# Kernel tuning notes

Measured on AMD Instinct MI355X. Metric: run time of the kernel, lower is better.

Reference implementation:

```python
import jax, jax.numpy as jnp
import numpy as np

B = 2; N_RAW = 16384; N_KP = 2048; M_VOX = 8192; C_VOX = 64
H_BEV, W_BEV, C_BEV, BEV_STRIDE = 200, 176, 256, 8
VOXEL_SIZE = np.array([0.05, 0.05, 0.1], np.float32)
PC_MIN = np.array([0.0, -40.0, -3.0], np.float32)
DOWNSAMPLE = 4
RAW_RADII = (0.4, 0.8); RAW_NS = (16, 16)
CONV_RADII = (1.2, 2.4); CONV_NS = (16, 32)
BN_SCALE = float(1.0 / np.sqrt(1.0 + 1e-5))  # eval-mode BN, running mean=0 var=1


def _fps_idx(pts, n):
    # farthest point sampling over pts [N,3] -> [n] int32 indices
    N = pts.shape[0]
    def step(carry, _):
        dists, last = carry
        d = jnp.sum((pts - pts[last]) ** 2, axis=-1)
        dists = jnp.minimum(dists, d)
        nxt = jnp.argmax(dists).astype(jnp.int32)
        return (dists, nxt), nxt
    init = (jnp.full((N,), 1e10, pts.dtype), jnp.int32(0))
    _, rest = jax.lax.scan(step, init, None, length=n - 1)
    return jnp.concatenate([jnp.zeros((1,), jnp.int32), rest])


def _bilinear(bev, x, y):
    # bev [H,W,C]; faithful to bilinear_interpolate_bev (clamp then weight)
    H, W, _ = bev.shape
    xf = jnp.floor(x); yf = jnp.floor(y)
    x0 = jnp.clip(xf.astype(jnp.int32), 0, W - 1)
    x1 = jnp.clip(xf.astype(jnp.int32) + 1, 0, W - 1)
    y0 = jnp.clip(yf.astype(jnp.int32), 0, H - 1)
    y1 = jnp.clip(yf.astype(jnp.int32) + 1, 0, H - 1)
    fa = bev[y1, x0]; fb = bev[y1, x1]; fc = bev[y0, x1]; fd = bev[y0, x0]
    x0f = x0.astype(x.dtype); x1f = x1.astype(x.dtype)
    y0f = y0.astype(y.dtype); y1f = y1.astype(y.dtype)
    wa = (x - x0f) * (y1f - y); wb = (x1f - x) * (y1f - y)
    wc = (x1f - x) * (y - y0f); wd = (x - x0f) * (y - y0f)
    return fd * wb[:, None] + fc * wa[:, None] + fa * wc[:, None] + fb * wd[:, None]


def _group(xyz, feats, new_xyz, radius, nsample):
    # ball query: first nsample points within radius (original order), pad with first hit
    M = xyz.shape[0]
    d2 = jnp.sum((new_xyz[:, None, :] - xyz[None, :, :]) ** 2, axis=-1)  # [K,M]
    mask = d2 < radius * radius
    key = jnp.where(mask, jnp.arange(M, dtype=jnp.int32)[None, :], M)
    idx = jnp.sort(key, axis=1)[:, :nsample]
    empty = ~jnp.any(mask, axis=1)
    idx = jnp.where(idx < M, idx, idx[:, :1])
    idx = jnp.clip(idx, 0, M - 1)
    g_xyz = xyz[idx] - new_xyz[:, None, :]
    g = jnp.concatenate([g_xyz, feats[idx]], axis=-1)  # [K,ns,3+C]
    return jnp.where(empty[:, None, None], 0.0, g), empty


def _bn_relu(x, g, b):
    return jax.nn.relu(x * (g * BN_SCALE) + b)


def _sa(xyz, feats, new_xyz, radii, nss, w0, g0, b0, w1, g1, b1):
    outs = []
    for i, (r, ns) in enumerate(zip(radii, nss)):
        grouped, empty = jax.vmap(lambda x, f, nx: _group(x, f, nx, r, ns))(xyz, feats, new_xyz)
        h = _bn_relu(grouped @ w0[i], g0[i], b0[i])
        h = _bn_relu(h @ w1[i], g1[i], b1[i])
        pooled = jnp.max(h, axis=2)  # [B,K,Cout]
        outs.append(jnp.where(empty[..., None], 0.0, pooled))
    return jnp.concatenate(outs, axis=-1)


def _forward(points, spatial_features, voxel_coords, voxel_features,
             raw_w0, raw_g0, raw_b0, raw_w1, raw_g1, raw_b1,
             conv_w0, conv_g0, conv_b0, conv_w1, conv_g1, conv_b1,
             fusion_w, fusion_g, fusion_b):
    pts = points.reshape(B, N_RAW, -1)
    xyz_raw = pts[..., 1:4]
    idxs = jax.vmap(lambda p: _fps_idx(p, N_KP))(jax.lax.stop_gradient(xyz_raw))
    kp = jnp.take_along_axis(xyz_raw, idxs[..., None], axis=1)  # [B,NKP,3]
    xi = (kp[..., 0] - PC_MIN[0]) / VOXEL_SIZE[0] / BEV_STRIDE
    yi = (kp[..., 1] - PC_MIN[1]) / VOXEL_SIZE[1] / BEV_STRIDE
    bev = jnp.transpose(spatial_features, (0, 2, 3, 1))  # [B,H,W,C]
    bev_feat = jax.vmap(_bilinear)(bev, xi, yi)  # [B,NKP,C_BEV]
    raw_feat = _sa(xyz_raw, pts[..., 4:], kp, RAW_RADII, RAW_NS,
                   raw_w0, raw_g0, raw_b0, raw_w1, raw_g1, raw_b1)
    vc = voxel_coords.reshape(B, M_VOX, 4)
    centers = (vc[..., jnp.array([3, 2, 1])].astype(jnp.float32) + 0.5) \
        * jnp.asarray(VOXEL_SIZE * DOWNSAMPLE) + jnp.asarray(PC_MIN)
    conv_feat = _sa(centers, voxel_features.reshape(B, M_VOX, C_VOX), kp, CONV_RADII, CONV_NS,
                    conv_w0, conv_g0, conv_b0, conv_w1, conv_g1, conv_b1)
    feats = jnp.concatenate([bev_feat, raw_feat, conv_feat], axis=-1).reshape(B * N_KP, -1)
    return _bn_relu(feats @ fusion_w, fusion_g, fusion_b)  # [B*NKP, 128]


def setup_inputs():
    key = jax.random.key(0)
    ks = jax.random.split(key, 8)
    xyz = jax.random.uniform(ks[0], (B * N_RAW, 3), jnp.float32) * jnp.array([70.4, 80.0, 4.0]) + jnp.array([0.0, -40.0, -3.0])
    inten = jax.random.uniform(ks[1], (B * N_RAW, 1), jnp.float32)
    bidx = jnp.repeat(jnp.arange(B, dtype=jnp.float32), N_RAW)[:, None]
    points = jnp.concatenate([bidx, xyz, inten], axis=1)
    spatial_features = jax.random.normal(ks[2], (B, C_BEV, H_BEV, W_BEV), jnp.float32)
    vb = jnp.repeat(jnp.arange(B, dtype=jnp.int32), M_VOX)[:, None]
    vz = jax.random.randint(ks[3], (B * M_VOX, 1), 0, 10, jnp.int32)
    vy = jax.random.randint(ks[4], (B * M_VOX, 1), 0, 400, jnp.int32)
    vx = jax.random.randint(ks[5], (B * M_VOX, 1), 0, 352, jnp.int32)
    voxel_coords = jnp.concatenate([vb, vz, vy, vx], axis=1)
    voxel_features = jax.random.normal(ks[6], (B * M_VOX, C_VOX), jnp.float32)
    pk = jax.random.split(ks[7], 5)
    w = lambda k, s: jax.random.normal(k, s, jnp.float32) * 0.05
    return dict(
        points=points, spatial_features=spatial_features,
        voxel_coords=voxel_coords, voxel_features=voxel_features,
        raw_w0=w(pk[0], (2, 4, 16)), raw_g0=jnp.ones((2, 16)), raw_b0=jnp.zeros((2, 16)),
        raw_w1=w(pk[1], (2, 16, 16)), raw_g1=jnp.ones((2, 16)), raw_b1=jnp.zeros((2, 16)),
        conv_w0=w(pk[2], (2, 67, 64)), conv_g0=jnp.ones((2, 64)), conv_b0=jnp.zeros((2, 64)),
        conv_w1=w(pk[3], (2, 64, 64)), conv_g1=jnp.ones((2, 64)), conv_b1=jnp.zeros((2, 64)),
        fusion_w=w(pk[4], (416, 128)), fusion_g=jnp.ones((128,)), fusion_b=jnp.zeros((128,)))


def reference(points, spatial_features, voxel_coords, voxel_features,
              raw_w0, raw_g0, raw_b0, raw_w1, raw_g1, raw_b1,
              conv_w0, conv_g0, conv_b0, conv_w1, conv_g1, conv_b1,
              fusion_w, fusion_g, fusion_b):
    return _forward(points, spatial_features, voxel_coords, voxel_features,
                    raw_w0, raw_g0, raw_b0, raw_w1, raw_g1, raw_b1,
                    conv_w0, conv_g0, conv_b0, conv_w1, conv_g1, conv_b1,
                    fusion_w, fusion_g, fusion_b)
```

## Files before the change

kernel.cpp:

```cpp
#include <hip/hip_runtime.h>


#define NRAW   16384
#define MVOX   8192
#define NKP    2048
#define NKPALL 4096

__device__ __constant__ float kBNS = (float)0.9999950000374997;

typedef float f32x2 __attribute__((ext_vector_type(2)));

__global__ __launch_bounds__(256) void prep_kernel(
    const float* __restrict__ pts, const int* __restrict__ vc,
    float4* __restrict__ xyz4, float4* __restrict__ cxyz4) {
#pragma clang fp contract(off)
  int i = blockIdx.x * 256 + threadIdx.x;
  if (i < 2 * NRAW) {
    const float* p = pts + (size_t)i * 5;
    xyz4[i] = make_float4(p[1], p[2], p[3], p[4]);
  }
  if (i < 2 * MVOX) {
    const int* v = vc + (size_t)i * 4;
    cxyz4[i] = make_float4(((float)v[3] + 0.5f) * 0.2f + 0.0f,
                           ((float)v[2] + 0.5f) * 0.2f + -40.0f,
                           ((float)v[1] + 0.5f) * 0.4f + -3.0f, 0.f);
  }
}

__global__ __launch_bounds__(1024) void sort_kernel(
    const float* __restrict__ pts, int* __restrict__ sperm) {
  const int b = blockIdx.x, t = threadIdx.x;
  __shared__ unsigned hist[256], cur[256];
  if (t < 256) hist[t] = 0u;
  __syncthreads();
  int bins[16];
#pragma unroll
  for (int k = 0; k < 16; ++k) {
    const int i = k * 1024 + t;
    const float y = pts[(size_t)(b * NRAW + i) * 5 + 2];
    int bin = (int)((y + 40.0f) * 3.2f);
    bin = bin < 0 ? 0 : (bin > 255 ? 255 : bin);
    bins[k] = bin;
    atomicAdd(&hist[bin], 1u);
  }
  __syncthreads();
  if (t == 0) {
    unsigned acc = 0;
    for (int i = 0; i < 256; ++i) { cur[i] = acc; acc += hist[i]; }
  }
  __syncthreads();
#pragma unroll
  for (int k = 0; k < 16; ++k) {
    const int i = k * 1024 + t;
    const unsigned pos = atomicAdd(&cur[bins[k]], 1u);
    sperm[b * NRAW + pos] = i;
  }
}

#define U64_STAGE(CTRL, RMASK)                                                 \
  {                                                                            \
    const unsigned tlo = (unsigned)__builtin_amdgcn_update_dpp(                \
        0, (int)lo, CTRL, RMASK, 0xf, true);                                   \
    const unsigned thi = (unsigned)__builtin_amdgcn_update_dpp(                \
        0, (int)hi, CTRL, RMASK, 0xf, true);                                   \
    const unsigned long long tv = ((unsigned long long)thi << 32) | tlo;       \
    const unsigned long long cv = ((unsigned long long)hi << 32) | lo;         \
    if (tv > cv) { hi = thi; lo = tlo; }                                       \
  }

__global__ __launch_bounds__(1024, 4) void fps_kernel(
    const int* __restrict__ sperm, const float4* __restrict__ xyz4,
    float* __restrict__ kx, float* __restrict__ ky, float* __restrict__ kz) {
#pragma clang fp contract(off)
  const int b = blockIdx.x;
  const int t = threadIdx.x;
  const int w = t >> 6, lane = t & 63;
  const int wb = w * 1024;
  const int base = b * NRAW;

  __shared__ unsigned long long slot[3];

  int pj[16];
  f32x2 px2[8], py2[8], pz2[8], dd2[8];
#pragma unroll
  for (int j = 0; j < 16; ++j)
    pj[j] = sperm[base + wb + j * 64 + lane];
#pragma unroll
  for (int j = 0; j < 16; ++j) {
    const float4 q = xyz4[base + pj[j]];
    px2[j >> 1][j & 1] = q.x;
    py2[j >> 1][j & 1] = q.y;
    pz2[j >> 1][j & 1] = q.z;
    dd2[j >> 1][j & 1] = 1e10f;
  }
  if (t < 3) slot[t] = 0ULL;

  float bnx = px2[0].x, bxx = px2[0].x, bny = py2[0].x, bxy = py2[0].x,
        bnz = pz2[0].x, bxz = pz2[0].x;
#pragma unroll
  for (int j = 1; j < 16; ++j) {
    bnx = fminf(bnx, px2[j >> 1][j & 1]); bxx = fmaxf(bxx, px2[j >> 1][j & 1]);
    bny = fminf(bny, py2[j >> 1][j & 1]); bxy = fmaxf(bxy, py2[j >> 1][j & 1]);
    bnz = fminf(bnz, pz2[j >> 1][j & 1]); bxz = fmaxf(bxz, pz2[j >> 1][j & 1]);
  }
#pragma unroll
  for (int off = 1; off < 64; off <<= 1) {
    bnx = fminf(bnx, __shfl_xor(bnx, off, 64));
    bxx = fmaxf(bxx, __shfl_xor(bxx, off, 64));
    bny = fminf(bny, __shfl_xor(bny, off, 64));
    bxy = fmaxf(bxy, __shfl_xor(bxy, off, 64));
    bnz = fminf(bnz, __shfl_xor(bnz, off, 64));
    bxz = fmaxf(bxz, __shfl_xor(bxz, off, 64));
  }

  const float4 p0 = xyz4[base];
  float lx = p0.x, ly = p0.y, lz = p0.z;
  if (t == 0) { kx[b * NKP] = lx; ky[b * NKP] = ly; kz[b * NKP] = lz; }

  unsigned long long cpk = 0ULL;
  float bvc = __builtin_inff();
  __syncthreads();

  for (int s = 1; s < NKP; ++s) {
    float dxm = fmaxf(fmaxf(bnx - lx, lx - bxx), 0.f);
    float dym = fmaxf(fmaxf(bny - ly, ly - bxy), 0.f);
    float dzm = fmaxf(fmaxf(bnz - lz, lz - bxz), 0.f);
    const float LB2 = dxm * dxm + dym * dym + dzm * dzm;
    if (!(LB2 * 0.9999f > bvc)) {
      const f32x2 lx2 = {lx, lx}, ly2 = {ly, ly}, lz2 = {lz, lz};
#pragma unroll
      for (int j8 = 0; j8 < 8; ++j8) {
        f32x2 dx = px2[j8] - lx2;
        f32x2 dy = py2[j8] - ly2;
        f32x2 dz = pz2[j8] - lz2;
        f32x2 d2 = dx * dx;
        d2 = d2 + dy * dy;
        d2 = d2 + dz * dz;
        dd2[j8] = __builtin_elementwise_min(dd2[j8], d2);
      }
      f32x2 t0 = __builtin_elementwise_max(dd2[0], dd2[1]);
      f32x2 t1 = __builtin_elementwise_max(dd2[2], dd2[3]);
      f32x2 t2 = __builtin_elementwise_max(dd2[4], dd2[5]);
      f32x2 t3 = __builtin_elementwise_max(dd2[6], dd2[7]);
      t0 = __builtin_elementwise_max(t0, t1);
      t2 = __builtin_elementwise_max(t2, t3);
      t0 = __builtin_elementwise_max(t0, t2);
      const float bv = fmaxf(t0.x, t0.y);
      const unsigned vb = __float_as_uint(bv);
      unsigned mo = 0xFFFFFFFFu;
#pragma unroll
      for (int j = 0; j < 16; ++j)
        if (__float_as_uint(dd2[j >> 1][j & 1]) == vb) {
          const unsigned o = (unsigned)pj[j];
          mo = o < mo ? o : mo;
        }
      unsigned hi = vb, lo = ~mo;
      U64_STAGE(0xB1,  0xf)
      U64_STAGE(0x4E,  0xf)
      U64_STAGE(0x124, 0xf)
      U64_STAGE(0x128, 0xf)
      U64_STAGE(0x142, 0xa)
      U64_STAGE(0x143, 0xc)
      bvc = __uint_as_float(
          (unsigned)__builtin_amdgcn_readlane((int)hi, 63));
      cpk = ((unsigned long long)hi << 32) | (unsigned long long)lo;
    }
    if (lane == 63) atomicMax(&slot[s % 3], cpk);
    __syncthreads();

    const unsigned long long g = slot[s % 3];
    const int wi = __builtin_amdgcn_readfirstlane((int)~(unsigned)g);
    if (t == 0) slot[(s + 2) % 3] = 0ULL;
    const float4 cw = xyz4[base + wi];
    lx = cw.x; ly = cw.y; lz = cw.z;
    if (t == 0) { kx[b * NKP + s] = lx; ky[b * NKP + s] = ly; kz[b * NKP + s] = lz; }
  }
}

__global__ __launch_bounds__(256) void bev_kernel(
    const float* __restrict__ sf, const float* __restrict__ kx,
    const float* __restrict__ ky, float* __restrict__ feats) {
#pragma clang fp contract(off)
  const int kidx = blockIdx.x;
  const int c = threadIdx.x;
  const int b = kidx >> 11;
  const float x = (kx[kidx] - 0.0f) / 0.05f / 8.0f;
  const float y = (ky[kidx] - (-40.0f)) / 0.05f / 8.0f;
  const float xf = floorf(x), yf = floorf(y);
  int x0 = (int)xf;     x0 = x0 < 0 ? 0 : (x0 > 175 ? 175 : x0);
  int x1 = (int)xf + 1; x1 = x1 < 0 ? 0 : (x1 > 175 ? 175 : x1);
  int y0 = (int)yf;     y0 = y0 < 0 ? 0 : (y0 > 199 ? 199 : y0);
  int y1 = (int)yf + 1; y1 = y1 < 0 ? 0 : (y1 > 199 ? 199 : y1);
  const float x0f = (float)x0, x1f = (float)x1, y0f = (float)y0, y1f = (float)y1;
  const float wa = (x - x0f) * (y1f - y);
  const float wb = (x1f - x) * (y1f - y);
  const float wc = (x1f - x) * (y - y0f);
  const float wd = (x - x0f) * (y - y0f);
  const float* base = sf + ((size_t)b * 256 + c) * (200 * 176);
  const float fa = base[y1 * 176 + x0];
  const float fb = base[y1 * 176 + x1];
  const float fc = base[y0 * 176 + x1];
  const float fd = base[y0 * 176 + x0];
  float r = fd * wb; r = r + fc * wa; r = r + fa * wc; r = r + fb * wd;
  feats[(size_t)kidx * 416 + c] = r;
}

__global__ __launch_bounds__(256) void raw_sa_kernel(
    const float4* __restrict__ xyz4,
    const float* __restrict__ kx, const float* __restrict__ ky,
    const float* __restrict__ kz,
    const float* __restrict__ w0, const float* __restrict__ g0,
    const float* __restrict__ b0, const float* __restrict__ w1,
    const float* __restrict__ g1, const float* __restrict__ b1,
    float* __restrict__ feats) {
  const int wv = threadIdx.x >> 6;
  const int lane = threadIdx.x & 63;
  const int gw = blockIdx.x * 4 + wv;
  const int ri = gw >> 12;
  const int kidx = gw & 4095;
  const int b = kidx >> 11;
  const float R2 = ri ? (float)(0.8 * 0.8) : (float)(0.4 * 0.4);

  __shared__ int   idxl[4][16];
  __shared__ float hbuf[4][16][17];

  const float kxv = kx[kidx], kyv = ky[kidx], kzv = kz[kidx];
  const int base = b * NRAW;
  int cnt = 0;
  {
#pragma clang fp contract(off)
    for (int ch = 0; ch < NRAW / 64 && cnt < 16; ++ch) {
      const float4 q = xyz4[base + ch * 64 + lane];
      float dx = kxv - q.x, dy = kyv - q.y, dz = kzv - q.z;
      float d2 = dx * dx; d2 = d2 + dy * dy; d2 = d2 + dz * dz;
      unsigned long long m = __ballot(d2 < R2);
      while (m && cnt < 16) {
        int bit = __builtin_ctzll(m);
        if (lane == 0) idxl[wv][cnt] = ch * 64 + bit;
        ++cnt;
        m &= m - 1;
      }
    }
  }
  const int outoff = kidx * 416 + 256 + ri * 16;
  if (cnt == 0) {
    if (lane < 16) feats[outoff + lane] = 0.f;
    return;
  }
  __threadfence_block();

  const int s = lane & 15, cq = lane >> 4;
  const int ss = (s < cnt) ? s : 0;
  const float4 q = xyz4[base + idxl[wv][ss]];
  const float gx = q.x - kxv, gy = q.y - kyv, gz = q.z - kzv, gi = q.w;
  const int wb0 = ri * 64, cb = ri * 16;
#pragma unroll
  for (int j = 0; j < 4; ++j) {
    int c = cq * 4 + j;
    float a = gx * w0[wb0 + c];
    a = fmaf(gy, w0[wb0 + 16 + c], a);
    a = fmaf(gz, w0[wb0 + 32 + c], a);
    a = fmaf(gi, w0[wb0 + 48 + c], a);
    a = fmaf(a, g0[cb + c] * kBNS, b0[cb + c]);
    hbuf[wv][s][c] = fmaxf(a, 0.f);
  }
  __threadfence_block();
  float o0 = 0.f, o1 = 0.f, o2 = 0.f, o3 = 0.f;
  const int wb1 = ri * 256;
#pragma unroll
  for (int k = 0; k < 16; ++k) {
    float hk = hbuf[wv][s][k];
    o0 = fmaf(hk, w1[wb1 + k * 16 + cq * 4 + 0], o0);
    o1 = fmaf(hk, w1[wb1 + k * 16 + cq * 4 + 1], o1);
    o2 = fmaf(hk, w1[wb1 + k * 16 + cq * 4 + 2], o2);
    o3 = fmaf(hk, w1[wb1 + k * 16 + cq * 4 + 3], o3);
  }
  float v0 = fmaxf(fmaf(o0, g1[cb + cq * 4 + 0] * kBNS, b1[cb + cq * 4 + 0]), 0.f);
  float v1 = fmaxf(fmaf(o1, g1[cb + cq * 4 + 1] * kBNS, b1[cb + cq * 4 + 1]), 0.f);
  float v2 = fmaxf(fmaf(o2, g1[cb + cq * 4 + 2] * kBNS, b1[cb + cq * 4 + 2]), 0.f);
  float v3 = fmaxf(fmaf(o3, g1[cb + cq * 4 + 3] * kBNS, b1[cb + cq * 4 + 3]), 0.f);
#pragma unroll
  for (int off = 1; off < 16; off <<= 1) {
    v0 = fmaxf(v0, __shfl_xor(v0, off, 64));
    v1 = fmaxf(v1, __shfl_xor(v1, off, 64));
    v2 = fmaxf(v2, __shfl_xor(v2, off, 64));
    v3 = fmaxf(v3, __shfl_xor(v3, off, 64));
  }
  if (s == 0) {
    feats[outoff + cq * 4 + 0] = v0;
    feats[outoff + cq * 4 + 1] = v1;
    feats[outoff + cq * 4 + 2] = v2;
    feats[outoff + cq * 4 + 3] = v3;
  }
}

__global__ __launch_bounds__(256) void conv_sa_kernel(
    const float4* __restrict__ cxyz4, const float* __restrict__ vf,
    const float* __restrict__ kx, const float* __restrict__ ky,
    const float* __restrict__ kz,
    const float* __restrict__ w0, const float* __restrict__ g0,
    const float* __restrict__ b0, const float* __restrict__ w1,
    const float* __restrict__ g1, const float* __restrict__ b1,
    float* __restrict__ feats) {
  const int wv = threadIdx.x >> 6;
  const int lane = threadIdx.x & 63;
  const int gw = blockIdx.x * 4 + wv;
  const int ri = gw >> 12;
  const int kidx = gw & 4095;
  const int b = kidx >> 11;
  const int NS = ri ? 32 : 16;
  const float R2 = ri ? (float)(2.4 * 2.4) : (float)(1.2 * 1.2);

  __shared__ int   idxl[4][32];
  __shared__ float gbuf[4][64];
  __shared__ float hbuf[4][32][64];

  const float kxv = kx[kidx], kyv = ky[kidx], kzv = kz[kidx];
  const int base = b * MVOX;
  int cnt = 0;
  {
#pragma clang fp contract(off)
    for (int ch = 0; ch < MVOX / 64 && cnt < NS; ++ch) {
      const float4 q = cxyz4[base + ch * 64 + lane];
      float dx = kxv - q.x, dy = kyv - q.y, dz = kzv - q.z;
      float d2 = dx * dx; d2 = d2 + dy * dy; d2 = d2 + dz * dz;
      unsigned long long m = __ballot(d2 < R2);
      while (m && cnt < NS) {
        int bit = __builtin_ctzll(m);
        if (lane == 0) idxl[wv][cnt] = ch * 64 + bit;
        ++cnt;
        m &= m - 1;
      }
    }
  }
  const int outoff = kidx * 416 + 288 + ri * 64;
  if (cnt == 0) {
    feats[outoff + lane] = 0.f;
    return;
  }
  __threadfence_block();

  const float wA0 = w0[(ri * 67 + 0) * 64 + lane];
  const float wA1 = w0[(ri * 67 + 1) * 64 + lane];
  const float wA2 = w0[(ri * 67 + 2) * 64 + lane];
  float wB[64];
#pragma unroll
  for (int k = 0; k < 64; ++k) wB[k] = w0[(ri * 67 + 3 + k) * 64 + lane];
  float wC[64];
#pragma unroll
  for (int k = 0; k < 64; ++k) wC[k] = w1[(ri * 64 + k) * 64 + lane];
  const float s0 = g0[ri * 64 + lane] * kBNS, bb0 = b0[ri * 64 + lane];
  const float s1 = g1[ri * 64 + lane] * kBNS, bb1 = b1[ri * 64 + lane];

  for (int sm = 0; sm < cnt; ++sm) {
    const int p = base + idxl[wv][sm];
    const float4 q = cxyz4[p];
    const float ox = q.x - kxv, oy = q.y - kyv, oz = q.z - kzv;
    gbuf[wv][lane] = vf[(size_t)p * 64 + lane];
    __threadfence_block();
    float acc = ox * wA0;
    acc = fmaf(oy, wA1, acc);
    acc = fmaf(oz, wA2, acc);
#pragma unroll
    for (int k4 = 0; k4 < 16; ++k4) {
      float4 g4 = *(const float4*)&gbuf[wv][k4 * 4];
      acc = fmaf(g4.x, wB[k4 * 4 + 0], acc);
      acc = fmaf(g4.y, wB[k4 * 4 + 1], acc);
      acc = fmaf(g4.z, wB[k4 * 4 + 2], acc);
      acc = fmaf(g4.w, wB[k4 * 4 + 3], acc);
    }
    hbuf[wv][sm][lane] = fmaxf(fmaf(acc, s0, bb0), 0.f);
    __threadfence_block();
  }
  float mx = -1e30f;
  for (int sm = 0; sm < cnt; ++sm) {
    float acc = 0.f;
#pragma unroll
    for (int k4 = 0; k4 < 16; ++k4) {
      float4 h4 = *(const float4*)&hbuf[wv][sm][k4 * 4];
      acc = fmaf(h4.x, wC[k4 * 4 + 0], acc);
      acc = fmaf(h4.y, wC[k4 * 4 + 1], acc);
      acc = fmaf(h4.z, wC[k4 * 4 + 2], acc);
      acc = fmaf(h4.w, wC[k4 * 4 + 3], acc);
    }
    mx = fmaxf(mx, fmaxf(fmaf(acc, s1, bb1), 0.f));
  }
  feats[outoff + lane] = mx;
}

__global__ __launch_bounds__(256) void fusion_kernel(
    const float* __restrict__ feats, const float* __restrict__ fw,
    const float* __restrict__ fg, const float* __restrict__ fb,
    float* __restrict__ out) {
  const int gid = blockIdx.x * 256 + threadIdx.x;
  const int kidx = gid >> 7, c = gid & 127;
  const float* f = feats + (size_t)kidx * 416;
  float acc = 0.f;
#pragma unroll 4
  for (int k = 0; k < 416; k += 4) {
    float4 fv = *(const float4*)(f + k);
    acc = fmaf(fv.x, fw[(k + 0) * 128 + c], acc);
    acc = fmaf(fv.y, fw[(k + 1) * 128 + c], acc);
    acc = fmaf(fv.z, fw[(k + 2) * 128 + c], acc);
    acc = fmaf(fv.w, fw[(k + 3) * 128 + c], acc);
  }
  out[gid] = fmaxf(fmaf(acc, fg[c] * kBNS, fb[c]), 0.f);
}

extern "C" void kernel_launch(void* const* d_in, const int* in_sizes, int n_in,
                              void* d_out, int out_size, void* d_ws, size_t ws_size,
                              hipStream_t stream) {
  (void)in_sizes; (void)n_in; (void)out_size; (void)ws_size;
  const float* pts = (const float*)d_in[0];
  const float* sf  = (const float*)d_in[1];
  const int*   vc  = (const int*)d_in[2];
  const float* vf  = (const float*)d_in[3];
  const float* raw_w0 = (const float*)d_in[4];
  const float* raw_g0 = (const float*)d_in[5];
  const float* raw_b0 = (const float*)d_in[6];
  const float* raw_w1 = (const float*)d_in[7];
  const float* raw_g1 = (const float*)d_in[8];
  const float* raw_b1 = (const float*)d_in[9];
  const float* conv_w0 = (const float*)d_in[10];
  const float* conv_g0 = (const float*)d_in[11];
  const float* conv_b0 = (const float*)d_in[12];
  const float* conv_w1 = (const float*)d_in[13];
  const float* conv_g1 = (const float*)d_in[14];
  const float* conv_b1 = (const float*)d_in[15];
  const float* fus_w = (const float*)d_in[16];
  const float* fus_g = (const float*)d_in[17];
  const float* fus_b = (const float*)d_in[18];
  float* out = (float*)d_out;

  float* W = (float*)d_ws;
  float4* xyz4  = (float4*)W;
  float4* cxyz4 = (float4*)(W + 131072);
  float* kx    = W + 196608;
  float* ky    = W + 200704;
  float* kz    = W + 204800;
  float* feats = W + 208896;
  int* sperm = (int*)(W + 208896);

  prep_kernel<<<128, 256, 0, stream>>>(pts, vc, xyz4, cxyz4);
  sort_kernel<<<2, 1024, 0, stream>>>(pts, sperm);
  fps_kernel<<<2, 1024, 0, stream>>>(sperm, xyz4, kx, ky, kz);
  bev_kernel<<<NKPALL, 256, 0, stream>>>(sf, kx, ky, feats);
  raw_sa_kernel<<<2048, 256, 0, stream>>>(xyz4, kx, ky, kz,
                                          raw_w0, raw_g0, raw_b0, raw_w1, raw_g1, raw_b1,
                                          feats);
  conv_sa_kernel<<<2048, 256, 0, stream>>>(cxyz4, vf, kx, ky, kz,
                                           conv_w0, conv_g0, conv_b0, conv_w1, conv_g1, conv_b1,
                                           feats);
  fusion_kernel<<<2048, 256, 0, stream>>>(feats, fus_w, fus_g, fus_b, out);
}
```

Baseline: 2.198 ms.

## Use y-binned sorted point lists to restrict ball-query scans in SA kernels

The sort kernel now also builds y-bin offset tables and y-sorted copies of raw point and voxel-center coordinates with their original indices. It is merged with the prep kernel, and voxels get the same treatment. Ball queries in raw_sa and conv_sa scan only the bins overlapping [y-R, y+R] instead of all points. Hits are then re-ordered into original index order with a wave-wide min selection, and the kernel falls back to the full linear scan when a window holds more than 64 hits. This targets the cost of scanning up to the whole point set per keypoint, at the price of running the prep work in only 2 blocks and adding extra workspace.

```diff
diff --git a/kernel.cpp b/kernel.cpp
--- a/kernel.cpp
+++ b/kernel.cpp
@@ -10,27 +10,39 @@
 
 typedef float f32x2 __attribute__((ext_vector_type(2)));
 
-__global__ __launch_bounds__(256) void prep_kernel(
+__device__ __forceinline__ unsigned wave_umax63(unsigned v) {
+  unsigned t;
+  t = (unsigned)__builtin_amdgcn_update_dpp(0, (int)v, 0xB1,  0xf, 0xf, true); v = v < t ? t : v;
+  t = (unsigned)__builtin_amdgcn_update_dpp(0, (int)v, 0x4E,  0xf, 0xf, true); v = v < t ? t : v;
+  t = (unsigned)__builtin_amdgcn_update_dpp(0, (int)v, 0x124, 0xf, 0xf, true); v = v < t ? t : v;
+  t = (unsigned)__builtin_amdgcn_update_dpp(0, (int)v, 0x128, 0xf, 0xf, true); v = v < t ? t : v;
+  t = (unsigned)__builtin_amdgcn_update_dpp(0, (int)v, 0x142, 0xa, 0xf, true); v = v < t ? t : v;
+  t = (unsigned)__builtin_amdgcn_update_dpp(0, (int)v, 0x143, 0xc, 0xf, true); v = v < t ? t : v;
+  return v;
+}
+
+__global__ __launch_bounds__(1024) void sort_prep_kernel(
     const float* __restrict__ pts, const int* __restrict__ vc,
-    float4* __restrict__ xyz4, float4* __restrict__ cxyz4) {
+    float4* __restrict__ xyz4, float4* __restrict__ cxyz4,
+    int* __restrict__ sperm, float4* __restrict__ xyzs,
+    int* __restrict__ pbin,
+    int* __restrict__ vsperm, float4* __restrict__ cxyzs,
+    int* __restrict__ vbin) {
 #pragma clang fp contract(off)
-  int i = blockIdx.x * 256 + threadIdx.x;
-  if (i < 2 * NRAW) {
-    const float* p = pts + (size_t)i * 5;
-    xyz4[i] = make_float4(p[1], p[2], p[3], p[4]);
-  }
-  if (i < 2 * MVOX) {
-    const int* v = vc + (size_t)i * 4;
-    cxyz4[i] = make_float4(((float)v[3] + 0.5f) * 0.2f + 0.0f,
-                           ((float)v[2] + 0.5f) * 0.2f + -40.0f,
-                           ((float)v[1] + 0.5f) * 0.4f + -3.0f, 0.f);
-  }
-}
-
-__global__ __launch_bounds__(1024) void sort_kernel(
-    const float* __restrict__ pts, int* __restrict__ sperm) {
   const int b = blockIdx.x, t = threadIdx.x;
+  for (int i = t; i < NRAW; i += 1024) {
+    const float* p = pts + (size_t)(b * NRAW + i) * 5;
+    xyz4[b * NRAW + i] = make_float4(p[1], p[2], p[3], p[4]);
+  }
+  for (int i = t; i < MVOX; i += 1024) {
+    const int* v = vc + (size_t)(b * MVOX + i) * 4;
+    cxyz4[b * MVOX + i] = make_float4(((float)v[3] + 0.5f) * 0.2f + 0.0f,
+                                      ((float)v[2] + 0.5f) * 0.2f + -40.0f,
+                                      ((float)v[1] + 0.5f) * 0.4f + -3.0f, 0.f);
+  }
+
   __shared__ unsigned hist[256], cur[256];
+
   if (t < 256) hist[t] = 0u;
   __syncthreads();
   int bins[16];
@@ -49,11 +61,50 @@
     for (int i = 0; i < 256; ++i) { cur[i] = acc; acc += hist[i]; }
   }
   __syncthreads();
+  if (t < 256) pbin[b * 257 + t] = (int)cur[t];
+  if (t == 0)  pbin[b * 257 + 256] = NRAW;
+  __syncthreads();
 #pragma unroll
   for (int k = 0; k < 16; ++k) {
     const int i = k * 1024 + t;
+    const float* p = pts + (size_t)(b * NRAW + i) * 5;
     const unsigned pos = atomicAdd(&cur[bins[k]], 1u);
     sperm[b * NRAW + pos] = i;
+    xyzs[b * NRAW + pos] = make_float4(p[1], p[2], p[3], p[4]);
+  }
+  __syncthreads();
+
+  if (t < 256) hist[t] = 0u;
+  __syncthreads();
+  int vbins[8];
+#pragma unroll
+  for (int k = 0; k < 8; ++k) {
+    const int i = k * 1024 + t;
+    const int* v = vc + (size_t)(b * MVOX + i) * 4;
+    const float cy = ((float)v[2] + 0.5f) * 0.2f + -40.0f;
+    int bin = (int)((cy + 40.0f) * 3.2f);
+    bin = bin < 0 ? 0 : (bin > 255 ? 255 : bin);
+    vbins[k] = bin;
+    atomicAdd(&hist[bin], 1u);
+  }
+  __syncthreads();
+  if (t == 0) {
+    unsigned acc = 0;
+    for (int i = 0; i < 256; ++i) { cur[i] = acc; acc += hist[i]; }
+  }
+  __syncthreads();
+  if (t < 256) vbin[b * 257 + t] = (int)cur[t];
+  if (t == 0)  vbin[b * 257 + 256] = MVOX;
+  __syncthreads();
+#pragma unroll
+  for (int k = 0; k < 8; ++k) {
+    const int i = k * 1024 + t;
+    const int* v = vc + (size_t)(b * MVOX + i) * 4;
+    const unsigned pos = atomicAdd(&cur[vbins[k]], 1u);
+    vsperm[b * MVOX + pos] = i;
+    cxyzs[b * MVOX + pos] = make_float4(((float)v[3] + 0.5f) * 0.2f + 0.0f,
+                                        ((float)v[2] + 0.5f) * 0.2f + -40.0f,
+                                        ((float)v[1] + 0.5f) * 0.4f + -3.0f, 0.f);
   }
 }
 
@@ -206,7 +257,8 @@
 }
 
 __global__ __launch_bounds__(256) void raw_sa_kernel(
-    const float4* __restrict__ xyz4,
+    const float4* __restrict__ xyz4, const float4* __restrict__ xyzs,
+    const int* __restrict__ sperm, const int* __restrict__ pbin,
     const float* __restrict__ kx, const float* __restrict__ ky,
     const float* __restrict__ kz,
     const float* __restrict__ w0, const float* __restrict__ g0,
@@ -219,28 +271,73 @@
   const int ri = gw >> 12;
   const int kidx = gw & 4095;
   const int b = kidx >> 11;
+  const float R  = ri ? 0.8f : 0.4f;
   const float R2 = ri ? (float)(0.8 * 0.8) : (float)(0.4 * 0.4);
 
-  __shared__ int   idxl[4][16];
+  __shared__ int   hlist[4][64];
   __shared__ float hbuf[4][16][17];
 
   const float kxv = kx[kidx], kyv = ky[kidx], kzv = kz[kidx];
   const int base = b * NRAW;
-  int cnt = 0;
+  int cnt = 0, hits = 0;
   {
 #pragma clang fp contract(off)
-    for (int ch = 0; ch < NRAW / 64 && cnt < 16; ++ch) {
-      const float4 q = xyz4[base + ch * 64 + lane];
-      float dx = kxv - q.x, dy = kyv - q.y, dz = kzv - q.z;
-      float d2 = dx * dx; d2 = d2 + dy * dy; d2 = d2 + dz * dz;
-      unsigned long long m = __ballot(d2 < R2);
-      while (m && cnt < 16) {
-        int bit = __builtin_ctzll(m);
-        if (lane == 0) idxl[wv][cnt] = ch * 64 + bit;
-        ++cnt;
-        m &= m - 1;
+    int b0i = (int)((kyv - R + 40.0f) * 3.2f) - 1;
+    b0i = b0i < 0 ? 0 : (b0i > 255 ? 255 : b0i);
+    int b1i = (int)((kyv + R + 40.0f) * 3.2f) + 1;
+    b1i = b1i < 0 ? 0 : (b1i > 255 ? 255 : b1i);
+    const int s0 = pbin[b * 257 + b0i];
+    const int s1 = pbin[b * 257 + b1i + 1];
+    if (s1 > s0) {
+      const int c0 = s0 >> 6, c1 = (s1 - 1) >> 6;
+      for (int ch = c0; ch <= c1; ++ch) {
+        const int pos = ch * 64 + lane;
+        const float4 q = xyzs[base + pos];
+        const int og = sperm[base + pos];
+        float dx = kxv - q.x, dy = kyv - q.y, dz = kzv - q.z;
+        float d2 = dx * dx; d2 = d2 + dy * dy; d2 = d2 + dz * dz;
+        const bool hit = (pos >= s0) && (pos < s1) && (d2 < R2);
+        unsigned long long m = __ballot(hit);
+        hits += __popcll(m);
+        while (m && cnt < 64) {
+          const int bit = __builtin_ctzll(m);
+          const int o = __shfl(og, bit, 64);
+          if (lane == 0) hlist[wv][cnt] = o;
+          ++cnt;
+          m &= m - 1;
+        }
       }
     }
+  }
+  if (hits > 64) {
+    cnt = 0;
+    {
+#pragma clang fp contract(off)
+      for (int ch = 0; ch < NRAW / 64 && cnt < 16; ++ch) {
+        const float4 q = xyz4[base + ch * 64 + lane];
+        float dx = kxv - q.x, dy = kyv - q.y, dz = kzv - q.z;
+        float d2 = dx * dx; d2 = d2 + dy * dy; d2 = d2 + dz * dz;
+        unsigned long long m = __ballot(d2 < R2);
+        while (m && cnt < 16) {
+          const int bit = __builtin_ctzll(m);
+          if (lane == 0) hlist[wv][cnt] = ch * 64 + bit;
+          ++cnt;
+          m &= m - 1;
+        }
+      }
+    }
+  } else if (hits > 16) {
+    __threadfence_block();
+    unsigned val = (lane < cnt) ? (unsigned)hlist[wv][lane] : 0xFFFFFFFFu;
+    for (int k = 0; k < 16; ++k) {
+      const unsigned mn =
+          ~(unsigned)__builtin_amdgcn_readlane((int)wave_umax63(~val), 63);
+      if (lane == 0) hlist[wv][k] = (int)mn;
+      if (val == mn) val = 0xFFFFFFFFu;
+    }
+    cnt = 16;
+  } else {
+    cnt = hits;
   }
   const int outoff = kidx * 416 + 256 + ri * 16;
   if (cnt == 0) {
@@ -251,7 +348,7 @@
 
   const int s = lane & 15, cq = lane >> 4;
   const int ss = (s < cnt) ? s : 0;
-  const float4 q = xyz4[base + idxl[wv][ss]];
+  const float4 q = xyz4[base + hlist[wv][ss]];
   const float gx = q.x - kxv, gy = q.y - kyv, gz = q.z - kzv, gi = q.w;
   const int wb0 = ri * 64, cb = ri * 16;
 #pragma unroll
@@ -295,7 +392,9 @@
 }
 
 __global__ __launch_bounds__(256) void conv_sa_kernel(
-    const float4* __restrict__ cxyz4, const float* __restrict__ vf,
+    const float4* __restrict__ cxyz4, const float4* __restrict__ cxyzs,
+    const int* __restrict__ vsperm, const int* __restrict__ vbin,
+    const float* __restrict__ vf,
     const float* __restrict__ kx, const float* __restrict__ ky,
     const float* __restrict__ kz,
     const float* __restrict__ w0, const float* __restrict__ g0,
@@ -309,29 +408,74 @@
   const int kidx = gw & 4095;
   const int b = kidx >> 11;
   const int NS = ri ? 32 : 16;
+  const float R  = ri ? 2.4f : 1.2f;
   const float R2 = ri ? (float)(2.4 * 2.4) : (float)(1.2 * 1.2);
 
-  __shared__ int   idxl[4][32];
+  __shared__ int   hlist[4][64];
   __shared__ float gbuf[4][64];
-  __shared__ float hbuf[4][32][64];
+  __shared__ float hbufC[4][32][64];
 
   const float kxv = kx[kidx], kyv = ky[kidx], kzv = kz[kidx];
   const int base = b * MVOX;
-  int cnt = 0;
+  int cnt = 0, hits = 0;
   {
 #pragma clang fp contract(off)
-    for (int ch = 0; ch < MVOX / 64 && cnt < NS; ++ch) {
-      const float4 q = cxyz4[base + ch * 64 + lane];
-      float dx = kxv - q.x, dy = kyv - q.y, dz = kzv - q.z;
-      float d2 = dx * dx; d2 = d2 + dy * dy; d2 = d2 + dz * dz;
-      unsigned long long m = __ballot(d2 < R2);
-      while (m && cnt < NS) {
-        int bit = __builtin_ctzll(m);
-        if (lane == 0) idxl[wv][cnt] = ch * 64 + bit;
-        ++cnt;
-        m &= m - 1;
+    int b0i = (int)((kyv - R + 40.0f) * 3.2f) - 1;
+    b0i = b0i < 0 ? 0 : (b0i > 255 ? 255 : b0i);
+    int b1i = (int)((kyv + R + 40.0f) * 3.2f) + 1;
+    b1i = b1i < 0 ? 0 : (b1i > 255 ? 255 : b1i);
+    const int s0 = vbin[b * 257 + b0i];
+    const int s1 = vbin[b * 257 + b1i + 1];
+    if (s1 > s0) {
+      const int c0 = s0 >> 6, c1 = (s1 - 1) >> 6;
+      for (int ch = c0; ch <= c1; ++ch) {
+        const int pos = ch * 64 + lane;
+        const float4 q = cxyzs[base + pos];
+        const int og = vsperm[base + pos];
+        float dx = kxv - q.x, dy = kyv - q.y, dz = kzv - q.z;
+        float d2 = dx * dx; d2 = d2 + dy * dy; d2 = d2 + dz * dz;
+        const bool hit = (pos >= s0) && (pos < s1) && (d2 < R2);
+        unsigned long long m = __ballot(hit);
+        hits += __popcll(m);
+        while (m && cnt < 64) {
+          const int bit = __builtin_ctzll(m);
+          const int o = __shfl(og, bit, 64);
+          if (lane == 0) hlist[wv][cnt] = o;
+          ++cnt;
+          m &= m - 1;
+        }
       }
     }
+  }
+  if (hits > 64) {
+    cnt = 0;
+    {
+#pragma clang fp contract(off)
+      for (int ch = 0; ch < MVOX / 64 && cnt < NS; ++ch) {
+        const float4 q = cxyz4[base + ch * 64 + lane];
+        float dx = kxv - q.x, dy = kyv - q.y, dz = kzv - q.z;
+        float d2 = dx * dx; d2 = d2 + dy * dy; d2 = d2 + dz * dz;
+        unsigned long long m = __ballot(d2 < R2);
+        while (m && cnt < NS) {
+          const int bit = __builtin_ctzll(m);
+          if (lane == 0) hlist[wv][cnt] = ch * 64 + bit;
+          ++cnt;
+          m &= m - 1;
+        }
+      }
+    }
+  } else if (hits > NS) {
+    __threadfence_block();
+    unsigned val = (lane < cnt) ? (unsigned)hlist[wv][lane] : 0xFFFFFFFFu;
+    for (int k = 0; k < NS; ++k) {
+      const unsigned mn =
+          ~(unsigned)__builtin_amdgcn_readlane((int)wave_umax63(~val), 63);
+      if (lane == 0) hlist[wv][k] = (int)mn;
+      if (val == mn) val = 0xFFFFFFFFu;
+    }
+    cnt = NS;
+  } else {
+    cnt = hits;
   }
   const int outoff = kidx * 416 + 288 + ri * 64;
   if (cnt == 0) {
@@ -353,7 +497,7 @@
   const float s1 = g1[ri * 64 + lane] * kBNS, bb1 = b1[ri * 64 + lane];
 
   for (int sm = 0; sm < cnt; ++sm) {
-    const int p = base + idxl[wv][sm];
+    const int p = base + hlist[wv][sm];
     const float4 q = cxyz4[p];
     const float ox = q.x - kxv, oy = q.y - kyv, oz = q.z - kzv;
     gbuf[wv][lane] = vf[(size_t)p * 64 + lane];
@@ -369,7 +513,7 @@
       acc = fmaf(g4.z, wB[k4 * 4 + 2], acc);
       acc = fmaf(g4.w, wB[k4 * 4 + 3], acc);
     }
-    hbuf[wv][sm][lane] = fmaxf(fmaf(acc, s0, bb0), 0.f);
+    hbufC[wv][sm][lane] = fmaxf(fmaf(acc, s0, bb0), 0.f);
     __threadfence_block();
   }
   float mx = -1e30f;
@@ -377,7 +521,7 @@
     float acc = 0.f;
 #pragma unroll
     for (int k4 = 0; k4 < 16; ++k4) {
-      float4 h4 = *(const float4*)&hbuf[wv][sm][k4 * 4];
+      float4 h4 = *(const float4*)&hbufC[wv][sm][k4 * 4];
       acc = fmaf(h4.x, wC[k4 * 4 + 0], acc);
       acc = fmaf(h4.y, wC[k4 * 4 + 1], acc);
       acc = fmaf(h4.z, wC[k4 * 4 + 2], acc);
@@ -435,20 +579,28 @@
   float* W = (float*)d_ws;
   float4* xyz4  = (float4*)W;
   float4* cxyz4 = (float4*)(W + 131072);
-  float* kx    = W + 196608;
-  float* ky    = W + 200704;
-  float* kz    = W + 204800;
-  float* feats = W + 208896;
-  int* sperm = (int*)(W + 208896);
-
-  prep_kernel<<<128, 256, 0, stream>>>(pts, vc, xyz4, cxyz4);
-  sort_kernel<<<2, 1024, 0, stream>>>(pts, sperm);
+  float* kx     = W + 196608;
+  float* ky     = W + 200704;
+  float* kz     = W + 204800;
+  float* feats  = W + 208896;
+  int*   sperm  = (int*)(W + 1912832);
+  float4* xyzs  = (float4*)(W + 1945600);
+  int*   vsperm = (int*)(W + 2076672);
+  float4* cxyzs = (float4*)(W + 2093056);
+  int*   pbin   = (int*)(W + 2158592);
+  int*   vbin   = (int*)(W + 2159106);
+
+  sort_prep_kernel<<<2, 1024, 0, stream>>>(pts, vc, xyz4, cxyz4,
+                                           sperm, xyzs, pbin,
+                                           vsperm, cxyzs, vbin);
   fps_kernel<<<2, 1024, 0, stream>>>(sperm, xyz4, kx, ky, kz);
   bev_kernel<<<NKPALL, 256, 0, stream>>>(sf, kx, ky, feats);
-  raw_sa_kernel<<<2048, 256, 0, stream>>>(xyz4, kx, ky, kz,
+  raw_sa_kernel<<<2048, 256, 0, stream>>>(xyz4, xyzs, sperm, pbin,
+                                          kx, ky, kz,
                                           raw_w0, raw_g0, raw_b0, raw_w1, raw_g1, raw_b1,
                                           feats);
-  conv_sa_kernel<<<2048, 256, 0, stream>>>(cxyz4, vf, kx, ky, kz,
+  conv_sa_kernel<<<2048, 256, 0, stream>>>(cxyz4, cxyzs, vsperm, vbin, vf,
+                                           kx, ky, kz,
                                            conv_w0, conv_g0, conv_b0, conv_w1, conv_g1, conv_b1,
                                            feats);
   fusion_kernel<<<2048, 256, 0, stream>>>(feats, fus_w, fus_g, fus_b, out);
```

New measurement: 2.033 ms. -7.5%, faster.
